# Kernel optimization log

Measured on AMD Instinct MI355X. Metric: run time of the kernel, lower is better.

Reference implementation:

```python
import jax, jax.numpy as jnp
import numpy as np

S, B, D, H, DFF = 1024, 8, 1024, 16, 4096
HD = D // H
EPS = 1e-5


def layernorm(x, g, b):
    m = jnp.mean(x, axis=-1, keepdims=True)
    v = jnp.mean(jnp.square(x - m), axis=-1, keepdims=True)
    return (x - m) * jax.lax.rsqrt(v + EPS) * g + b


def setup_inputs() -> dict:
    key = jax.random.key(0)
    ks = jax.random.split(key, 6)
    w = 0.02
    return {
        "src": jax.random.normal(ks[0], (S, B, D), dtype=jnp.float32),
        "in_proj_w": jax.random.normal(ks[1], (3 * D, D), dtype=jnp.float32) * w,
        "in_proj_b": jnp.zeros((3 * D,), dtype=jnp.float32),
        "out_w": jax.random.normal(ks[2], (D, D), dtype=jnp.float32) * w,
        "out_b": jnp.zeros((D,), dtype=jnp.float32),
        "lin1_w": jax.random.normal(ks[3], (DFF, D), dtype=jnp.float32) * w,
        "lin1_b": jnp.zeros((DFF,), dtype=jnp.float32),
        "lin2_w": jax.random.normal(ks[4], (D, DFF), dtype=jnp.float32) * w,
        "lin2_b": jnp.zeros((D,), dtype=jnp.float32),
        "n1_g": jnp.ones((D,), dtype=jnp.float32),
        "n1_b": jnp.zeros((D,), dtype=jnp.float32),
        "n2_g": jnp.ones((D,), dtype=jnp.float32),
        "n2_b": jnp.zeros((D,), dtype=jnp.float32),
    }


def reference(src, in_proj_w, in_proj_b, out_w, out_b,
              lin1_w, lin1_b, lin2_w, lin2_b,
              n1_g, n1_b, n2_g, n2_b):
    # self-attention block (eval mode: dropout = identity)
    qkv = jnp.einsum('sbd,ed->sbe', src, in_proj_w) + in_proj_b  # [S,B,3D]
    q, k, v = jnp.split(qkv, 3, axis=-1)
    q = q.reshape(S, B, H, HD) * (1.0 / np.sqrt(HD)).astype(np.float32)
    k = k.reshape(S, B, H, HD)
    v = v.reshape(S, B, H, HD)
    scores = jnp.einsum('sbhd,tbhd->bhst', q, k)        # [B,H,S,S]
    attn = jax.nn.softmax(scores, axis=-1)
    o = jnp.einsum('bhst,tbhd->sbhd', attn, v).reshape(S, B, D)
    o = jnp.einsum('sbd,ed->sbe', o, out_w) + out_b
    # post-LN residuals
    x = layernorm(src + o, n1_g, n1_b)
    h = jax.nn.relu(jnp.einsum('sbd,fd->sbf', x, lin1_w) + lin1_b)
    f = jnp.einsum('sbf,df->sbd', h, lin2_w) + lin2_b
    return layernorm(x + f, n2_g, n2_b)
```

## Files before the change

### kernel.cpp

```cpp
#include <hip/hip_runtime.h>
#include <cstdint>
#include <cstddef>

#define S_  1024
#define B_  8
#define D_  1024
#define H_  16
#define HD_ 64
#define DFF_ 4096
#define M_  (S_*B_)
#define QKV_N (3*D_)

typedef float f32x4 __attribute__((ext_vector_type(4)));
typedef __bf16 bf16x8 __attribute__((ext_vector_type(8)));
typedef __bf16 bf16x4 __attribute__((ext_vector_type(4)));

#define GLDS16(gp, lp) __builtin_amdgcn_global_load_lds( \
    (__attribute__((address_space(1))) void*)(gp), \
    (__attribute__((address_space(3))) void*)(lp), 16, 0, 0)

#define CB0 (M_*D_/4)
#define CB1 (CB0 + QKV_N*D_/4)
#define CB2 (CB1 + D_*D_/4)
#define CB3 (CB2 + DFF_*D_/4)
#define CB4 (CB3 + D_*DFF_/4)

__global__ __launch_bounds__(256)
void cvt_all(const float* __restrict__ src, const float* __restrict__ w1f,
             const float* __restrict__ w2f, const float* __restrict__ w3f,
             const float* __restrict__ w4f,
             __bf16* __restrict__ src_bf, __bf16* __restrict__ w1,
             __bf16* __restrict__ w2, __bf16* __restrict__ w3,
             __bf16* __restrict__ w4)
{
    int i = blockIdx.x * 256 + threadIdx.x;
    const float* in; __bf16* out; int off;
    if      (i < CB0) { in = src; out = src_bf; off = 0;   }
    else if (i < CB1) { in = w1f; out = w1;     off = CB0; }
    else if (i < CB2) { in = w2f; out = w2;     off = CB1; }
    else if (i < CB3) { in = w3f; out = w3;     off = CB2; }
    else if (i < CB4) { in = w4f; out = w4;     off = CB3; }
    else return;
    int j = i - off;
    float4 v = *(const float4*)(in + (size_t)j * 4);
    __bf16 t[4] = {(__bf16)v.x, (__bf16)v.y, (__bf16)v.z, (__bf16)v.w};
    *(uint2*)(out + (size_t)j * 4) = *(uint2*)t;
}

template<bool OUT_BF16, bool RELU, bool ADD_BIAS, bool SPLITZ>
__global__ __launch_bounds__(512, 2)
void gemm256(const __bf16* __restrict__ A, const __bf16* __restrict__ W,
             const float* __restrict__ bias,
             void* __restrict__ Cv0, void* __restrict__ Cv1,
             int N, int Kloop, int lda)
{
    extern __shared__ __bf16 lds[];
    __bf16* As = lds;
    __bf16* Bs = lds + 3 * 8192;

    const int tid  = threadIdx.x;
    const int lane = tid & 63;
    const int wv   = tid >> 6;
    const int quad = lane >> 4;
    const int l15  = lane & 15;
    const int wm   = (wv >> 2) * 128;
    const int wn   = (wv & 3) * 64;

    int id  = blockIdx.y * gridDim.x + blockIdx.x;
    int nwg = gridDim.x * gridDim.y;
    int q8  = nwg >> 3;
    int swz = (id & 7) * q8 + (id >> 3);
    const int m0 = (swz % gridDim.x) * 256;
    const int n0 = (swz / gridDim.x) * 256;

    void* Cv = Cv0;
    if (SPLITZ) {
        const int koff = blockIdx.z * Kloop;
        A += koff;
        W += koff;
        if (blockIdx.z) Cv = Cv1;
    }

    const int nt = Kloop >> 5;

    #define STAGE(kt, buf) do { \
        const int k0s = (kt) << 5; \
        _Pragma("unroll") \
        for (int u = 0; u < 2; ++u) { \
            int c = u * 512 + tid; \
            int row = c >> 2, sl = c & 3; \
            GLDS16(A + (size_t)(m0 + row) * lda + k0s + sl * 8, \
                   (char*)(As + (buf) * 8192) + c * 16); \
            GLDS16(W + (size_t)(n0 + row) * lda + k0s + sl * 8, \
                   (char*)(Bs + (buf) * 8192) + c * 16); \
        } \
    } while (0)

    STAGE(0, 0);
    STAGE(1, 1);
    asm volatile("s_waitcnt vmcnt(4)" ::: "memory");
    __builtin_amdgcn_s_barrier();
    __builtin_amdgcn_sched_barrier(0);

    f32x4 acc[8][4] = {};

    int cur = 0, stg = 2;
    for (int t = 0; t < nt; ++t) {
        if (t + 2 < nt) STAGE(t + 2, stg);

        bf16x8 bf[4], af[8];
        #pragma unroll
        for (int j = 0; j < 4; ++j)
            bf[j] = *(const bf16x8*)(Bs + cur * 8192 + (wn + j * 16 + l15) * 32 + quad * 8);
        #pragma unroll
        for (int i = 0; i < 8; ++i)
            af[i] = *(const bf16x8*)(As + cur * 8192 + (wm + i * 16 + l15) * 32 + quad * 8);

        __builtin_amdgcn_s_setprio(1);
        #pragma unroll
        for (int i = 0; i < 8; ++i)
            #pragma unroll
            for (int j = 0; j < 4; ++j)
                acc[i][j] = __builtin_amdgcn_mfma_f32_16x16x32_bf16(af[i], bf[j], acc[i][j], 0, 0, 0);
        __builtin_amdgcn_s_setprio(0);

        if (t + 1 < nt) {
            if (t + 2 < nt) { asm volatile("s_waitcnt vmcnt(4)" ::: "memory"); }
            else            { asm volatile("s_waitcnt vmcnt(0)" ::: "memory"); }
            __builtin_amdgcn_s_barrier();
            __builtin_amdgcn_sched_barrier(0);
        }
        if (++cur == 3) cur = 0;
        if (++stg == 3) stg = 0;
    }
    #undef STAGE

    #pragma unroll
    for (int j = 0; j < 4; ++j) {
        const int col = n0 + wn + j * 16 + l15;
        const float bv = ADD_BIAS ? bias[col] : 0.f;
        #pragma unroll
        for (int i = 0; i < 8; ++i) {
            const int rbase = m0 + wm + i * 16 + quad * 4;
            #pragma unroll
            for (int r = 0; r < 4; ++r) {
                float v = acc[i][j][r] + bv;
                if (RELU) v = fmaxf(v, 0.f);
                if (OUT_BF16)
                    ((__bf16*)Cv)[(size_t)(rbase + r) * N + col] = (__bf16)v;
                else
                    ((float*)Cv)[(size_t)(rbase + r) * N + col] = v;
            }
        }
    }
}

__global__ __launch_bounds__(256)
void v_transpose(const __bf16* __restrict__ qkv, __bf16* __restrict__ vt)
{
    __shared__ __bf16 T[64 * 65];
    const int tid = threadIdx.x;
    const int t0  = blockIdx.x * 64;
    const int bh  = blockIdx.y;
    const int b   = bh & (B_ - 1);
    const int h   = bh / B_;

    #pragma unroll
    for (int j = 0; j < 2; ++j) {
        int c = j * 256 + tid;
        int i = c >> 3, cc = c & 7;
        const __bf16* g = qkv + (size_t)((t0 + i) * B_ + b) * QKV_N + 2 * D_ + h * HD_ + cc * 8;
        bf16x8 v = *(const bf16x8*)g;
        #pragma unroll
        for (int u = 0; u < 8; ++u) T[(cc * 8 + u) * 65 + i] = v[u];
    }
    __syncthreads();
    #pragma unroll
    for (int j = 0; j < 2; ++j) {
        int c = j * 256 + tid;
        int d = c >> 3, cc = c & 7;
        __bf16 pk[8];
        #pragma unroll
        for (int u = 0; u < 8; ++u) pk[u] = T[d * 65 + cc * 8 + u];
        *(uint4*)(vt + ((size_t)bh * HD_ + d) * S_ + t0 + cc * 8) = *(uint4*)pk;
    }
}

#define TST 72

__global__ __launch_bounds__(256)
void attn_flash(const __bf16* __restrict__ qkv, const __bf16* __restrict__ vt,
                __bf16* __restrict__ out)
{
    __shared__ __bf16 Qs[64 * TST];
    __shared__ __bf16 Ks[64 * TST];
    __shared__ __bf16 Vt[64 * TST];
    __shared__ __bf16 Ps[64 * TST];

    const int tid  = threadIdx.x;
    const int lane = tid & 63;
    const int wv   = tid >> 6;
    const int quad = lane >> 4;
    const int l15  = lane & 15;
    const int s0 = blockIdx.x * 64;
    const int bh = blockIdx.y;
    const int b  = bh & (B_ - 1);
    const int h  = bh / B_;

    #pragma unroll
    for (int j = 0; j < 2; ++j) {
        int c = j * 256 + tid;
        int i = c >> 3, cc = c & 7;
        const __bf16* g = qkv + (size_t)((s0 + i) * B_ + b) * QKV_N + h * HD_ + cc * 8;
        *(uint4*)(Qs + i * TST + cc * 8) = *(const uint4*)g;
    }

    f32x4 oacc[4] = {};
    float m_run = -1e30f, l_run = 0.f;
    const float C2    = 0.125f * 1.44269504f;
    const float LOG2E = 1.44269504f;

    for (int t0 = 0; t0 < S_; t0 += 64) {
        __syncthreads();
        #pragma unroll
        for (int j = 0; j < 2; ++j) {
            int c = j * 256 + tid;
            int i = c >> 3, cc = c & 7;
            const __bf16* g = qkv + (size_t)((t0 + i) * B_ + b) * QKV_N + D_ + h * HD_ + cc * 8;
            *(uint4*)(Ks + i * TST + cc * 8) = *(const uint4*)g;
        }
        #pragma unroll
        for (int j = 0; j < 2; ++j) {
            int c = j * 256 + tid;
            int d = c >> 3, cc = c & 7;
            const __bf16* g = vt + ((size_t)bh * HD_ + d) * S_ + t0 + cc * 8;
            *(uint4*)(Vt + d * TST + cc * 8) = *(const uint4*)g;
        }
        __syncthreads();

        f32x4 sacc[4] = {};
        #pragma unroll
        for (int kk = 0; kk < 2; ++kk) {
            bf16x8 bq = *(const bf16x8*)(Qs + (wv * 16 + l15) * TST + kk * 32 + quad * 8);
            #pragma unroll
            for (int j = 0; j < 4; ++j) {
                bf16x8 ak = *(const bf16x8*)(Ks + (j * 16 + l15) * TST + kk * 32 + quad * 8);
                sacc[j] = __builtin_amdgcn_mfma_f32_16x16x32_bf16(ak, bq, sacc[j], 0, 0, 0);
            }
        }

        float mx = sacc[0][0];
        #pragma unroll
        for (int j = 0; j < 4; ++j)
            #pragma unroll
            for (int r = 0; r < 4; ++r) mx = fmaxf(mx, sacc[j][r]);
        mx = fmaxf(mx, __shfl_xor(mx, 16, 64));
        mx = fmaxf(mx, __shfl_xor(mx, 32, 64));
        float mnew = fmaxf(m_run, mx * 0.125f);
        float k1 = mnew * LOG2E;
        float rs = 0.f;
        #pragma unroll
        for (int j = 0; j < 4; ++j)
            #pragma unroll
            for (int r = 0; r < 4; ++r) {
                float p = __builtin_amdgcn_exp2f(sacc[j][r] * C2 - k1);
                sacc[j][r] = p;
                rs += p;
            }
        rs += __shfl_xor(rs, 16, 64);
        rs += __shfl_xor(rs, 32, 64);
        float alpha = __builtin_amdgcn_exp2f((m_run - mnew) * LOG2E);
        l_run = l_run * alpha + rs;
        m_run = mnew;

        #pragma unroll
        for (int j = 0; j < 4; ++j) {
            __bf16 pk[4] = {(__bf16)sacc[j][0], (__bf16)sacc[j][1],
                            (__bf16)sacc[j][2], (__bf16)sacc[j][3]};
            *(uint2*)(Ps + (wv * 16 + l15) * TST + j * 16 + quad * 4) = *(uint2*)pk;
        }

        #pragma unroll
        for (int r = 0; r < 4; ++r) {
            float ar = __shfl(alpha, quad * 4 + r, 64);
            #pragma unroll
            for (int jd = 0; jd < 4; ++jd) oacc[jd][r] *= ar;
        }

        #pragma unroll
        for (int kk = 0; kk < 2; ++kk) {
            bf16x8 ap = *(const bf16x8*)(Ps + (wv * 16 + l15) * TST + kk * 32 + quad * 8);
            #pragma unroll
            for (int jd = 0; jd < 4; ++jd) {
                bf16x8 bv = *(const bf16x8*)(Vt + (jd * 16 + l15) * TST + kk * 32 + quad * 8);
                oacc[jd] = __builtin_amdgcn_mfma_f32_16x16x32_bf16(ap, bv, oacc[jd], 0, 0, 0);
            }
        }
    }

    float linv = 1.f / l_run;
    #pragma unroll
    for (int r = 0; r < 4; ++r) {
        float lr = __shfl(linv, quad * 4 + r, 64);
        int s = s0 + wv * 16 + quad * 4 + r;
        #pragma unroll
        for (int jd = 0; jd < 4; ++jd) {
            int d = jd * 16 + l15;
            out[(size_t)(s * B_ + b) * D_ + h * HD_ + d] = (__bf16)(oacc[jd][r] * lr);
        }
    }
}

__global__ __launch_bounds__(256)
void ln_res3(const float* __restrict__ xa, const __bf16* __restrict__ p0,
             const __bf16* __restrict__ p1, const float* __restrict__ bias,
             const float* __restrict__ g, const float* __restrict__ beta,
             float* __restrict__ yout, __bf16* __restrict__ ybf)
{
    __shared__ float red[8];
    const int row = blockIdx.x;
    const int tid = threadIdx.x;
    const size_t base = (size_t)row * D_ + tid * 4;

    float4 a  = *(const float4*)(xa + base);
    bf16x4 q0 = *(const bf16x4*)(p0 + base);
    bf16x4 q1 = *(const bf16x4*)(p1 + base);
    float4 bb = *(const float4*)(bias + tid * 4);
    float x0 = a.x + (float)q0[0] + (float)q1[0] + bb.x;
    float x1 = a.y + (float)q0[1] + (float)q1[1] + bb.y;
    float x2 = a.z + (float)q0[2] + (float)q1[2] + bb.z;
    float x3 = a.w + (float)q0[3] + (float)q1[3] + bb.w;

    float s  = x0 + x1 + x2 + x3;
    float ss = x0 * x0 + x1 * x1 + x2 * x2 + x3 * x3;
    for (int msk = 1; msk <= 32; msk <<= 1) {
        s  += __shfl_xor(s,  msk, 64);
        ss += __shfl_xor(ss, msk, 64);
    }
    const int wv = tid >> 6;
    if ((tid & 63) == 0) { red[wv] = s; red[4 + wv] = ss; }
    __syncthreads();
    s  = red[0] + red[1] + red[2] + red[3];
    ss = red[4] + red[5] + red[6] + red[7];
    float mean = s * (1.f / D_);
    float var  = ss * (1.f / D_) - mean * mean;
    float rstd = rsqrtf(var + 1e-5f);

    float4 gv = *(const float4*)(g + tid * 4);
    float4 bv = *(const float4*)(beta + tid * 4);
    float y0 = (x0 - mean) * rstd * gv.x + bv.x;
    float y1 = (x1 - mean) * rstd * gv.y + bv.y;
    float y2 = (x2 - mean) * rstd * gv.z + bv.z;
    float y3 = (x3 - mean) * rstd * gv.w + bv.w;
    *(float4*)(yout + base) = make_float4(y0, y1, y2, y3);
    if (ybf) {
        __bf16 t[4] = {(__bf16)y0, (__bf16)y1, (__bf16)y2, (__bf16)y3};
        *(uint2*)(ybf + base) = *(uint2*)t;
    }
}

extern "C" void kernel_launch(void* const* d_in, const int* in_sizes, int n_in,
                              void* d_out, int out_size, void* d_ws, size_t ws_size,
                              hipStream_t stream)
{
    const float* src       = (const float*)d_in[0];
    const float* in_proj_w = (const float*)d_in[1];
    const float* in_proj_b = (const float*)d_in[2];
    const float* out_w     = (const float*)d_in[3];
    const float* out_b     = (const float*)d_in[4];
    const float* lin1_w    = (const float*)d_in[5];
    const float* lin1_b    = (const float*)d_in[6];
    const float* lin2_w    = (const float*)d_in[7];
    const float* lin2_b    = (const float*)d_in[8];
    const float* n1_g = (const float*)d_in[9];
    const float* n1_b = (const float*)d_in[10];
    const float* n2_g = (const float*)d_in[11];
    const float* n2_b = (const float*)d_in[12];

    char* ws = (char*)d_ws;
    size_t off = 0;
    auto alloc = [&](size_t bytes) { char* p = ws + off; off += (bytes + 255) & ~(size_t)255; return p; };

    __bf16* src_bf = (__bf16*)alloc((size_t)M_ * D_ * 2);
    __bf16* w1     = (__bf16*)alloc((size_t)QKV_N * D_ * 2);
    __bf16* w2     = (__bf16*)alloc((size_t)D_ * D_ * 2);
    __bf16* w3     = (__bf16*)alloc((size_t)DFF_ * D_ * 2);
    __bf16* w4     = (__bf16*)alloc((size_t)D_ * DFF_ * 2);
    __bf16* qkv    = (__bf16*)alloc((size_t)M_ * QKV_N * 2);
    char*   h_r    = alloc((size_t)M_ * DFF_ * 2);
    __bf16* xbf    = (__bf16*)alloc((size_t)M_ * D_ * 2);
    float*  xf     = (float*)alloc((size_t)M_ * D_ * 4);
    __bf16* vt     = (__bf16*)alloc((size_t)B_ * H_ * HD_ * S_ * 2);

    const size_t PART = (size_t)M_ * D_;
    __bf16* attn_o = src_bf;
    __bf16* o0 = (__bf16*)h_r;
    __bf16* o1 = o0 + PART;
    __bf16* hbf = (__bf16*)h_r;
    __bf16* f0 = vt;
    __bf16* f1 = xbf;

    const size_t SHM = 3 * 2 * 8192 * sizeof(__bf16);

    cvt_all<<<(CB4 + 255) / 256, 256, 0, stream>>>(
        src, in_proj_w, out_w, lin1_w, lin2_w, src_bf, w1, w2, w3, w4);

    gemm256<true, false, true, false><<<dim3(M_ / 256, QKV_N / 256), 512, SHM, stream>>>(
        src_bf, w1, in_proj_b, qkv, nullptr, QKV_N, D_, D_);

    v_transpose<<<dim3(S_ / 64, B_ * H_), 256, 0, stream>>>(qkv, vt);

    attn_flash<<<dim3(S_ / 64, B_ * H_), 256, 0, stream>>>(qkv, vt, attn_o);

    gemm256<true, false, false, true><<<dim3(M_ / 256, D_ / 256, 2), 512, SHM, stream>>>(
        attn_o, w2, nullptr, o0, o1, D_, D_ / 2, D_);

    ln_res3<<<M_, 256, 0, stream>>>(src, o0, o1, out_b, n1_g, n1_b, xf, xbf);

    gemm256<true, true, true, false><<<dim3(M_ / 256, DFF_ / 256), 512, SHM, stream>>>(
        xbf, w3, lin1_b, hbf, nullptr, DFF_, D_, D_);

    gemm256<true, false, false, true><<<dim3(M_ / 256, D_ / 256, 2), 512, SHM, stream>>>(
        hbf, w4, nullptr, f0, f1, D_, DFF_ / 2, DFF_);

    ln_res3<<<M_, 256, 0, stream>>>(xf, f0, f1, lin2_b, n2_g, n2_b, (float*)d_out, nullptr);
}
```

Measured before the change: 529.7 us.

## Swizzle GEMM LDS layout, group tiles for L2 reuse, remap attention blocks

XOR-swizzles the 16-byte slot index within each 32-element LDS row of the GEMM tiles, applied both when staging via global_load_lds and when reading MFMA fragments, to reduce LDS bank conflicts. Remaps GEMM workgroups into 8x4 tile chunks after the XCD-aware interleave so neighbouring blocks share A/W panels in cache. Reorders the epilogue loops so bias is loaded once per column and stores iterate over j innermost. Remaps attention blocks so the 16 query tiles of one (b,h) sit on the same XCD, improving K/V reuse. The chunk mapping assumes gridDim.x is a multiple of 8 and the tile count is a multiple of 32.

```diff
diff --git a/kernel.cpp b/kernel.cpp
--- a/kernel.cpp
+++ b/kernel.cpp
@@ -66,12 +66,17 @@
     const int wm   = (wv >> 2) * 128;
     const int wn   = (wv & 3) * 64;
 
-    int id  = blockIdx.y * gridDim.x + blockIdx.x;
-    int nwg = gridDim.x * gridDim.y;
-    int q8  = nwg >> 3;
-    int swz = (id & 7) * q8 + (id >> 3);
-    const int m0 = (swz % gridDim.x) * 256;
-    const int n0 = (swz / gridDim.x) * 256;
+    const int id  = blockIdx.y * gridDim.x + blockIdx.x;
+    const int nwg = gridDim.x * gridDim.y;
+    const int q8  = nwg >> 3;
+    const int k   = (id & 7) * q8 + (id >> 3);
+    const int within = k & 31;
+    const int chunk  = k >> 5;
+    const int nchm   = gridDim.x >> 3;
+    const int cm     = chunk % nchm;
+    const int cn     = chunk / nchm;
+    const int m0 = (cm * 8 + (within & 7)) * 256;
+    const int n0 = (cn * 4 + (within >> 3)) * 256;
 
     void* Cv = Cv0;
     if (SPLITZ) {
@@ -87,11 +92,12 @@
         const int k0s = (kt) << 5; \
         _Pragma("unroll") \
         for (int u = 0; u < 2; ++u) { \
-            int c = u * 512 + tid; \
-            int row = c >> 2, sl = c & 3; \
-            GLDS16(A + (size_t)(m0 + row) * lda + k0s + sl * 8, \
+            int c   = u * 512 + tid; \
+            int row = c >> 2; \
+            int ssl = (c & 3) ^ ((row >> 1) & 3); \
+            GLDS16(A + (size_t)(m0 + row) * lda + k0s + ssl * 8, \
                    (char*)(As + (buf) * 8192) + c * 16); \
-            GLDS16(W + (size_t)(n0 + row) * lda + k0s + sl * 8, \
+            GLDS16(W + (size_t)(n0 + row) * lda + k0s + ssl * 8, \
                    (char*)(Bs + (buf) * 8192) + c * 16); \
         } \
     } while (0)
@@ -110,11 +116,15 @@
 
         bf16x8 bf[4], af[8];
         #pragma unroll
-        for (int j = 0; j < 4; ++j)
-            bf[j] = *(const bf16x8*)(Bs + cur * 8192 + (wn + j * 16 + l15) * 32 + quad * 8);
-        #pragma unroll
-        for (int i = 0; i < 8; ++i)
-            af[i] = *(const bf16x8*)(As + cur * 8192 + (wm + i * 16 + l15) * 32 + quad * 8);
+        for (int j = 0; j < 4; ++j) {
+            int rb = wn + j * 16 + l15;
+            bf[j] = *(const bf16x8*)(Bs + cur * 8192 + rb * 32 + (quad ^ ((rb >> 1) & 3)) * 8);
+        }
+        #pragma unroll
+        for (int i = 0; i < 8; ++i) {
+            int ra = wm + i * 16 + l15;
+            af[i] = *(const bf16x8*)(As + cur * 8192 + ra * 32 + (quad ^ ((ra >> 1) & 3)) * 8);
+        }
 
         __builtin_amdgcn_s_setprio(1);
         #pragma unroll
@@ -135,16 +145,19 @@
     }
     #undef STAGE
 
-    #pragma unroll
-    for (int j = 0; j < 4; ++j) {
-        const int col = n0 + wn + j * 16 + l15;
-        const float bv = ADD_BIAS ? bias[col] : 0.f;
-        #pragma unroll
-        for (int i = 0; i < 8; ++i) {
-            const int rbase = m0 + wm + i * 16 + quad * 4;
-            #pragma unroll
-            for (int r = 0; r < 4; ++r) {
-                float v = acc[i][j][r] + bv;
+    float bvj[4];
+    #pragma unroll
+    for (int j = 0; j < 4; ++j)
+        bvj[j] = ADD_BIAS ? bias[n0 + wn + j * 16 + l15] : 0.f;
+    #pragma unroll
+    for (int i = 0; i < 8; ++i) {
+        const int rbase = m0 + wm + i * 16 + quad * 4;
+        #pragma unroll
+        for (int r = 0; r < 4; ++r) {
+            #pragma unroll
+            for (int j = 0; j < 4; ++j) {
+                const int col = n0 + wn + j * 16 + l15;
+                float v = acc[i][j][r] + bvj[j];
                 if (RELU) v = fmaxf(v, 0.f);
                 if (OUT_BF16)
                     ((__bf16*)Cv)[(size_t)(rbase + r) * N + col] = (__bf16)v;
@@ -202,8 +215,11 @@
     const int wv   = tid >> 6;
     const int quad = lane >> 4;
     const int l15  = lane & 15;
-    const int s0 = blockIdx.x * 64;
-    const int bh = blockIdx.y;
+
+    const int id = blockIdx.y * gridDim.x + blockIdx.x;
+    const int k  = (id & 7) * ((S_ / 64) * B_ * H_ / 8) + (id >> 3);
+    const int s0 = (k & 15) * 64;
+    const int bh = k >> 4;
     const int b  = bh & (B_ - 1);
     const int h  = bh / B_;
 
```

Result: faster. 495.7 us (-6.4%).
